# Kernel tuning notes

Hardware: AMD Instinct MI355X
Metric: run time of the kernel (lower is better)

## Reference

```python
import jax, jax.numpy as jnp
import numpy as np

H = 1024      # hidden_size
M = 64        # matrix_dim = int(sqrt(4096))
R = 2         # rank
LS = 2048     # local_size = budget_size // 2


def setup_inputs() -> dict:
    key = jax.random.key(0)
    ks = jax.random.split(key, 12)
    B, S = 4, 2048
    def lin(k, fan_in, fan_out):
        # stored as [in, out] so forward is x @ W
        return jax.random.normal(k, (fan_in, fan_out), dtype=jnp.float32) / np.sqrt(fan_in)
    return {
        "x": jax.random.normal(ks[0], (B, S, H), dtype=jnp.float32),
        "W_decay": lin(ks[1], H, 1),
        "W_key": lin(ks[2], H, R * M),
        "W_value": lin(ks[3], H, R * M),
        "W_ql": lin(ks[4], H, M),
        "W_qr": lin(ks[5], H, M),
        "W_rec_out": lin(ks[6], M, H),
        "W_up": lin(ks[7], H, LS),
        "W_gate": lin(ks[8], H, LS),
        "W_down": lin(ks[9], LS, H),
        "init_state": jnp.zeros((M, M), dtype=jnp.float32),
    }


def reference(x, W_decay, W_key, W_value, W_ql, W_qr, W_rec_out, W_up, W_gate, W_down, init_state):
    B, S, _ = x.shape
    # Precompute all per-token projections (vectorized over batch & seq)
    decay = jax.nn.sigmoid(x @ W_decay)[..., 0]            # [B,S]
    keys = (x @ W_key).reshape(B, S, R, M)                 # [B,S,R,M]
    values = (x @ W_value).reshape(B, S, R, M)             # [B,S,R,M]
    write = jnp.einsum('bsrm,bsrn->bsmn', keys, values) / float(R)  # [B,S,M,M]
    ql = x @ W_ql                                          # [B,S,M]
    qr = x @ W_qr                                          # [B,S,M]

    def step(state, inp):
        d, w, ql_t, qr_t = inp                             # d:[B], w:[B,M,M], ql/qr:[B,M]
        d3 = d[:, None, None]
        state = d3 * state + (1.0 - d3) * w                # decayed matrix-state update
        read = jnp.einsum('bm,bmn->bn', ql_t, state) * qr_t  # [B,M]
        return state, read

    state0 = jnp.broadcast_to(init_state, (B, M, M))
    # scan over time axis (time-major inputs)
    _, reads = jax.lax.scan(
        step, state0,
        (decay.transpose(1, 0), write.transpose(1, 0, 2, 3),
         ql.transpose(1, 0, 2), qr.transpose(1, 0, 2)))
    reads = reads.transpose(1, 0, 2)                       # [B,S,M]

    recurrent = jax.nn.silu(reads) @ W_rec_out             # [B,S,H]
    local = ((x @ W_up) * jax.nn.silu(x @ W_gate)) @ W_down  # SwiGLU branch
    return recurrent + local
```

## Files before the change

kernel.cpp:

```cpp
#include <hip/hip_runtime.h>
#include <hip/hip_bf16.h>

typedef __bf16 bf16x8 __attribute__((ext_vector_type(8)));
typedef float f32x4 __attribute__((ext_vector_type(4)));

#define BS   8192
#define Hd   1024
#define LSd  2048
#define Md   64

static __device__ __forceinline__ float bfu2f(unsigned short u) {
  return __uint_as_float(((unsigned int)u) << 16);
}
static __device__ __forceinline__ __hip_bfloat16 f2bf(float f) { return __float2bfloat16(f); }



__global__ __launch_bounds__(256) void conv_frag_kernel(const float* __restrict__ src,
    __hip_bfloat16* __restrict__ dst) {
  int wid = (blockIdx.x * 256 + threadIdx.x) >> 6;
  int lane = threadIdx.x & 63;
  int t = wid >> 3, ri = wid & 7;
  int mb = t >> 5, kt = t & 31;
  int row = mb * 128 + ri * 16 + (lane & 15);
  int k = kt * 32 + (lane >> 4) * 8;
  const float* s = src + (size_t)row * 1024 + k;
  float4 f0 = *(const float4*)s;
  float4 f1 = *(const float4*)(s + 4);
  union { unsigned short u8[8]; uint4 v; } o;
  o.u8[0] = __bfloat16_as_ushort(f2bf(f0.x)); o.u8[1] = __bfloat16_as_ushort(f2bf(f0.y));
  o.u8[2] = __bfloat16_as_ushort(f2bf(f0.z)); o.u8[3] = __bfloat16_as_ushort(f2bf(f0.w));
  o.u8[4] = __bfloat16_as_ushort(f2bf(f1.x)); o.u8[5] = __bfloat16_as_ushort(f2bf(f1.y));
  o.u8[6] = __bfloat16_as_ushort(f2bf(f1.z)); o.u8[7] = __bfloat16_as_ushort(f2bf(f1.w));
  *(uint4*)(dst + (size_t)wid * 512 + lane * 8) = o.v;
}

__global__ __launch_bounds__(256) void prep_wcat_frag_kernel(const float* __restrict__ Wd,
    const float* __restrict__ Wk, const float* __restrict__ Wv,
    const float* __restrict__ Wql, const float* __restrict__ Wqr,
    __hip_bfloat16* __restrict__ out) {
  int i = blockIdx.x * 256 + threadIdx.x;
  int t = i >> 12, ri = (i >> 9) & 7, l = (i >> 3) & 63, e = i & 7;
  int n = (t >> 5) * 128 + ri * 16 + (l & 15);
  int h = (t & 31) * 32 + (l >> 4) * 8 + e;
  float v = 0.f;
  if (n == 0)        v = Wd[h];
  else if (n < 129)  v = Wk[h * 128 + (n - 1)];
  else if (n < 257)  v = Wv[h * 128 + (n - 129)];
  else if (n < 321)  v = Wql[h * 64 + (n - 257)];
  else if (n < 385)  v = Wqr[h * 64 + (n - 321)];
  out[i] = f2bf(v);
}

__global__ __launch_bounds__(256) void transpose_all_kernel(
    const float* __restrict__ Wup, const float* __restrict__ Wgate,
    const float* __restrict__ Wdown, const float* __restrict__ Wrec,
    __hip_bfloat16* __restrict__ Wug_f, __hip_bfloat16* __restrict__ Wdn_f,
    __hip_bfloat16* __restrict__ Wrc_f) {
  __shared__ float tile[32][129];
  int b = blockIdx.x;
  const float* src; __hip_bfloat16* dst; int Ktot, Nsrc, n_off, kt, nb;
  if (b < 512)        { src = Wup;   dst = Wug_f; Ktot = 1024; Nsrc = 2048; n_off = 0;    int r = b;        kt = r & 31; nb = r >> 5; }
  else if (b < 1024)  { src = Wgate; dst = Wug_f; Ktot = 1024; Nsrc = 2048; n_off = 2048; int r = b - 512;  kt = r & 31; nb = r >> 5; }
  else if (b < 1536)  { src = Wdown; dst = Wdn_f; Ktot = 2048; Nsrc = 1024; n_off = 0;    int r = b - 1024; kt = r & 63; nb = r >> 6; }
  else                { src = Wrec;  dst = Wrc_f; Ktot = 64;   Nsrc = 1024; n_off = 0;    int r = b - 1536; kt = r & 1;  nb = r >> 1; }
  int k0 = kt * 32, n0 = nb * 128;
  int tid = threadIdx.x;
  int kr = tid >> 3, nc = (tid & 7) * 16;
  const float* s = src + (size_t)(k0 + kr) * Nsrc + n0 + nc;
  #pragma unroll
  for (int u = 0; u < 16; u += 4) {
    float4 f = *(const float4*)(s + u);
    tile[kr][nc + u + 0] = f.x; tile[kr][nc + u + 1] = f.y;
    tile[kr][nc + u + 2] = f.z; tile[kr][nc + u + 3] = f.w;
  }
  __syncthreads();
  int wave = tid >> 6, lane = tid & 63;
  int tIdx = ((n0 + n_off) >> 7) * (Ktot >> 5) + kt;
  __hip_bfloat16* d = dst + ((size_t)tIdx << 12);
  #pragma unroll
  for (int it = 0; it < 2; ++it) {
    int ri = wave * 2 + it;
    int nl = ri * 16 + (lane & 15), kq = (lane >> 4) * 8;
    union { unsigned short u8[8]; uint4 v; } o;
    #pragma unroll
    for (int e = 0; e < 8; ++e)
      o.u8[e] = __bfloat16_as_ushort(f2bf(tile[kq + e][nl]));
    *(uint4*)(d + ri * 512 + lane * 8) = o.v;
  }
}


static __device__ __forceinline__ void stage_async_frag(const __hip_bfloat16* __restrict__ tile_src,
    __hip_bfloat16* __restrict__ dst, int wave, int lane) {
  #pragma unroll
  for (int it = 0; it < 2; ++it) {
    int ri = wave * 2 + it;
    __builtin_amdgcn_global_load_lds(
        (const __attribute__((address_space(1))) void*)(tile_src + ri * 512 + lane * 8),
        (__attribute__((address_space(3))) void*)(dst + ri * 512),
        16, 0, 0);
  }
}

static __device__ __forceinline__ void mfma_single(const __hip_bfloat16* sA, const __hip_bfloat16* sB,
    int wm16, int wn16, int lane, f32x4 acc[4][4]) {
  bf16x8 af[4], bg[4];
  #pragma unroll
  for (int i = 0; i < 4; ++i) af[i] = *(const bf16x8*)(sA + (wm16 + i) * 512 + lane * 8);
  #pragma unroll
  for (int j = 0; j < 4; ++j) bg[j] = *(const bf16x8*)(sB + (wn16 + j) * 512 + lane * 8);
  #pragma unroll
  for (int i = 0; i < 4; ++i)
    #pragma unroll
    for (int j = 0; j < 4; ++j)
      acc[i][j] = __builtin_amdgcn_mfma_f32_16x16x32_bf16(af[i], bg[j], acc[i][j], 0, 0, 0);
}

static __device__ __forceinline__ void mfma_dual(const __hip_bfloat16* sA,
    const __hip_bfloat16* sBu, const __hip_bfloat16* sBg,
    int wm16, int wn16, int lane, f32x4 accu[4][4], f32x4 accg[4][4]) {
  bf16x8 af[4], bu[4], bg[4];
  #pragma unroll
  for (int i = 0; i < 4; ++i) af[i] = *(const bf16x8*)(sA + (wm16 + i) * 512 + lane * 8);
  #pragma unroll
  for (int j = 0; j < 4; ++j) bu[j] = *(const bf16x8*)(sBu + (wn16 + j) * 512 + lane * 8);
  #pragma unroll
  for (int j = 0; j < 4; ++j) bg[j] = *(const bf16x8*)(sBg + (wn16 + j) * 512 + lane * 8);
  #pragma unroll
  for (int i = 0; i < 4; ++i)
    #pragma unroll
    for (int j = 0; j < 4; ++j) {
      accu[i][j] = __builtin_amdgcn_mfma_f32_16x16x32_bf16(af[i], bu[j], accu[i][j], 0, 0, 0);
      accg[i][j] = __builtin_amdgcn_mfma_f32_16x16x32_bf16(af[i], bg[j], accg[i][j], 0, 0, 0);
    }
}

__global__ __launch_bounds__(256, 2) void gemm_proj_kernel(const __hip_bfloat16* __restrict__ A,
    const __hip_bfloat16* __restrict__ Bt, float* __restrict__ C) {
  __shared__ __align__(16) __hip_bfloat16 sA[8192];
  __shared__ __align__(16) __hip_bfloat16 sB[8192];
  int tid = threadIdx.x, mb = blockIdx.x, nb = blockIdx.y;
  int wave = tid >> 6, lane = tid & 63;
  int wm16 = (wave >> 1) * 4, wn16 = (wave & 1) * 4;
  int fr = lane & 15, q4 = (lane >> 4) * 4;
  f32x4 acc[4][4] = {};
  for (int kt = 0; kt < 32; kt += 2) {
    __syncthreads();
    stage_async_frag(A + ((size_t)(mb * 32 + kt) << 12), sA, wave, lane);
    stage_async_frag(A + ((size_t)(mb * 32 + kt + 1) << 12), sA + 4096, wave, lane);
    stage_async_frag(Bt + ((size_t)(nb * 32 + kt) << 12), sB, wave, lane);
    stage_async_frag(Bt + ((size_t)(nb * 32 + kt + 1) << 12), sB + 4096, wave, lane);
    __syncthreads();
    mfma_single(sA, sB, wm16, wn16, lane, acc);
    mfma_single(sA + 4096, sB + 4096, wm16, wn16, lane, acc);
  }
  #pragma unroll
  for (int i = 0; i < 4; ++i)
    #pragma unroll
    for (int j = 0; j < 4; ++j) {
      int row = mb * 128 + (wm16 + i) * 16 + q4;
      int col = nb * 128 + (wn16 + j) * 16 + fr;
      #pragma unroll
      for (int rg = 0; rg < 4; ++rg)
        C[(size_t)(row + rg) * 512 + col] = acc[i][j][rg];
    }
}

__global__ __launch_bounds__(256, 2) void gemm_upgate_kernel(const __hip_bfloat16* __restrict__ A,
    const __hip_bfloat16* __restrict__ Bt, __hip_bfloat16* __restrict__ hout) {
  __shared__ __align__(16) __hip_bfloat16 sA[8192];
  __shared__ __align__(16) __hip_bfloat16 sBu[8192];
  __shared__ __align__(16) __hip_bfloat16 sBg[8192];
  int tid = threadIdx.x, mb = blockIdx.x, nb = blockIdx.y;
  int wave = tid >> 6, lane = tid & 63;
  int wm16 = (wave >> 1) * 4, wn16 = (wave & 1) * 4;
  int fr = lane & 15, q4 = (lane >> 4) * 4;
  f32x4 accu[4][4] = {}, accg[4][4] = {};
  for (int kt = 0; kt < 32; kt += 2) {
    __syncthreads();
    stage_async_frag(A + ((size_t)(mb * 32 + kt) << 12), sA, wave, lane);
    stage_async_frag(A + ((size_t)(mb * 32 + kt + 1) << 12), sA + 4096, wave, lane);
    stage_async_frag(Bt + ((size_t)(nb * 32 + kt) << 12), sBu, wave, lane);
    stage_async_frag(Bt + ((size_t)(nb * 32 + kt + 1) << 12), sBu + 4096, wave, lane);
    stage_async_frag(Bt + ((size_t)((nb + 16) * 32 + kt) << 12), sBg, wave, lane);
    stage_async_frag(Bt + ((size_t)((nb + 16) * 32 + kt + 1) << 12), sBg + 4096, wave, lane);
    __syncthreads();
    mfma_dual(sA, sBu, sBg, wm16, wn16, lane, accu, accg);
    mfma_dual(sA + 4096, sBu + 4096, sBg + 4096, wm16, wn16, lane, accu, accg);
  }
  #pragma unroll
  for (int i = 0; i < 4; ++i)
    #pragma unroll
    for (int j = 0; j < 4; ++j) {
      int col = nb * 128 + (wn16 + j) * 16 + fr;
      int q = (col >> 3) & 3, e = col & 7;
      size_t base = ((size_t)(mb * 64 + (col >> 5)) << 12) + (wm16 + i) * 512 + q * 128 + e;
      #pragma unroll
      for (int rg = 0; rg < 4; ++rg) {
        float u = accu[i][j][rg], g = accg[i][j][rg];
        float hv = u * g / (1.f + __expf(-g));
        hout[base + (q4 + rg) * 8] = f2bf(hv);
      }
    }
}

__global__ __launch_bounds__(256, 2) void gemm_final_kernel(const __hip_bfloat16* __restrict__ A,
    const __hip_bfloat16* __restrict__ Bt, const __hip_bfloat16* __restrict__ A2,
    const __hip_bfloat16* __restrict__ B2t, float* __restrict__ C) {
  __shared__ __align__(16) __hip_bfloat16 sA[8192];
  __shared__ __align__(16) __hip_bfloat16 sB[8192];
  int tid = threadIdx.x, mb = blockIdx.x, nb = blockIdx.y;
  int wave = tid >> 6, lane = tid & 63;
  int wm16 = (wave >> 1) * 4, wn16 = (wave & 1) * 4;
  int fr = lane & 15, q4 = (lane >> 4) * 4;
  f32x4 acc[4][4] = {};
  for (int kt = 0; kt < 64; kt += 2) {
    __syncthreads();
    stage_async_frag(A + ((size_t)(mb * 64 + kt) << 12), sA, wave, lane);
    stage_async_frag(A + ((size_t)(mb * 64 + kt + 1) << 12), sA + 4096, wave, lane);
    stage_async_frag(Bt + ((size_t)(nb * 64 + kt) << 12), sB, wave, lane);
    stage_async_frag(Bt + ((size_t)(nb * 64 + kt + 1) << 12), sB + 4096, wave, lane);
    __syncthreads();
    mfma_single(sA, sB, wm16, wn16, lane, acc);
    mfma_single(sA + 4096, sB + 4096, wm16, wn16, lane, acc);
  }
  {
    __syncthreads();
    stage_async_frag(A2 + ((size_t)(mb * 2) << 12), sA, wave, lane);
    stage_async_frag(A2 + ((size_t)(mb * 2 + 1) << 12), sA + 4096, wave, lane);
    stage_async_frag(B2t + ((size_t)(nb * 2) << 12), sB, wave, lane);
    stage_async_frag(B2t + ((size_t)(nb * 2 + 1) << 12), sB + 4096, wave, lane);
    __syncthreads();
    mfma_single(sA, sB, wm16, wn16, lane, acc);
    mfma_single(sA + 4096, sB + 4096, wm16, wn16, lane, acc);
  }
  #pragma unroll
  for (int i = 0; i < 4; ++i)
    #pragma unroll
    for (int j = 0; j < 4; ++j) {
      int row = mb * 128 + (wm16 + i) * 16 + q4;
      int col = nb * 128 + (wn16 + j) * 16 + fr;
      #pragma unroll
      for (int rg = 0; rg < 4; ++rg)
        C[(size_t)(row + rg) * Hd + col] = acc[i][j][rg];
    }
}


__global__ __launch_bounds__(256) void scan_chunk_kernel(const float* __restrict__ proj,
    float* __restrict__ Lam, float* __restrict__ udv, float* __restrict__ alpha,
    float* __restrict__ dS) {
  int bc = blockIdx.x, t0 = bc * 64, tid = threadIdx.x;
  __shared__ float d_s[64], ld_s[64], Lam_s[64], u_s[64];
  __shared__ __align__(16) __hip_bfloat16 k_s[128 * 64];
  __shared__ __align__(16) __hip_bfloat16 v_s[128 * 64];
  if (tid < 64) {
    float z = proj[(size_t)(t0 + tid) * 512];
    float dd = 1.f / (1.f + __expf(-z));
    float l = (z >= 0.f) ? -log1pf(__expf(-z)) : (z - log1pf(__expf(z)));
    d_s[tid] = dd; ld_s[tid] = l;
  }
  __syncthreads();
  if (tid == 0) {
    float s = 0.f;
    for (int j = 0; j < 64; ++j) { s += ld_s[j]; Lam_s[j] = s; }
  }
  __syncthreads();
  float Lend = Lam_s[63];
  if (tid < 64) {
    u_s[tid] = (1.f - d_s[tid]) * __expf(Lend - Lam_s[tid]) * 0.5f;
    Lam[t0 + tid] = Lam_s[tid];
    udv[t0 + tid] = (1.f - d_s[tid]) * 0.5f;
  }
  if (tid == 0) alpha[bc] = __expf(Lend);
  __syncthreads();
  for (int i = tid; i < 128 * 64; i += 256) {
    int jr = i >> 6, m = i & 63, j = jr >> 1, r = jr & 1;
    const float* rowp = proj + (size_t)(t0 + j) * 512;
    k_s[i] = f2bf(u_s[j] * rowp[1 + r * 64 + m]);
    v_s[i] = f2bf(rowp[129 + r * 64 + m]);
  }
  __syncthreads();
  int m0 = (tid & 15) * 4, n0 = (tid >> 4) * 4;
  float acc[4][4] = {{0.f}};
  for (int jr = 0; jr < 128; ++jr) {
    ushort4 ku = *(const ushort4*)&k_s[jr * 64 + m0];
    ushort4 vu = *(const ushort4*)&v_s[jr * 64 + n0];
    float k0 = bfu2f(ku.x), k1 = bfu2f(ku.y), k2 = bfu2f(ku.z), k3 = bfu2f(ku.w);
    float v0 = bfu2f(vu.x), v1 = bfu2f(vu.y), v2 = bfu2f(vu.z), v3 = bfu2f(vu.w);
    acc[0][0] += k0 * v0; acc[0][1] += k0 * v1; acc[0][2] += k0 * v2; acc[0][3] += k0 * v3;
    acc[1][0] += k1 * v0; acc[1][1] += k1 * v1; acc[1][2] += k1 * v2; acc[1][3] += k1 * v3;
    acc[2][0] += k2 * v0; acc[2][1] += k2 * v1; acc[2][2] += k2 * v2; acc[2][3] += k2 * v3;
    acc[3][0] += k3 * v0; acc[3][1] += k3 * v1; acc[3][2] += k3 * v2; acc[3][3] += k3 * v3;
  }
  float* outp = dS + (size_t)bc * 4096;
  #pragma unroll
  for (int a = 0; a < 4; ++a)
    #pragma unroll
    for (int b2 = 0; b2 < 4; ++b2)
      outp[(m0 + a) * 64 + (n0 + b2)] = acc[a][b2];
}

__global__ __launch_bounds__(256) void scan_cross_kernel(const float* __restrict__ dS,
    const float* __restrict__ alpha, const float* __restrict__ init_state,
    float* __restrict__ Sin) {
  int idx = blockIdx.x * 256 + threadIdx.x;
  int b = idx >> 12, e = idx & 4095;
  float s = init_state[e];
  for (int c = 0; c < 32; ++c) {
    int bc = b * 32 + c;
    Sin[(size_t)bc * 4096 + e] = s;
    s = alpha[bc] * s + dS[(size_t)bc * 4096 + e];
  }
}

#define QLD 68

__global__ __launch_bounds__(256) void scan_read_kernel(const float* __restrict__ proj,
    const float* __restrict__ Lam, const float* __restrict__ udv,
    const float* __restrict__ Sin, __hip_bfloat16* __restrict__ Rd) {
  int bc = blockIdx.x, t0 = bc * 64, tid = threadIdx.x;
  __shared__ __align__(16) __hip_bfloat16 ql_s[64 * QLD];
  __shared__ __align__(16) __hip_bfloat16 kv_s[128 * 64];
  __shared__ __align__(16) __hip_bfloat16 S_s[64 * 64];
  __shared__ __align__(16) __hip_bfloat16 P_s[128 * 64];
  __shared__ float Lam_s[64], ud_s[64], eL_s[64];
  for (int i = tid; i < 64 * 64; i += 256) {
    int t = i >> 6, m = i & 63;
    ql_s[t * QLD + m] = f2bf(proj[(size_t)(t0 + t) * 512 + 257 + m]);
    S_s[i] = f2bf(Sin[(size_t)bc * 4096 + i]);
  }
  for (int i = tid; i < 128 * 64; i += 256) {
    int jr = i >> 6, m = i & 63, j = jr >> 1, r = jr & 1;
    kv_s[i] = f2bf(proj[(size_t)(t0 + j) * 512 + 1 + r * 64 + m]);
  }
  if (tid < 64) {
    float L = Lam[t0 + tid];
    Lam_s[tid] = L; ud_s[tid] = udv[t0 + tid]; eL_s[tid] = __expf(L);
  }
  __syncthreads();
  int tr = (tid & 15) * 4, n0 = (tid >> 4) * 4;
  float acc[4][4] = {{0.f}};
  for (int mb4 = 0; mb4 < 64; mb4 += 4) {
    float sm[4][4];
    #pragma unroll
    for (int mm = 0; mm < 4; ++mm) {
      ushort4 sv = *(const ushort4*)&S_s[(mb4 + mm) * 64 + n0];
      sm[mm][0] = bfu2f(sv.x); sm[mm][1] = bfu2f(sv.y);
      sm[mm][2] = bfu2f(sv.z); sm[mm][3] = bfu2f(sv.w);
    }
    #pragma unroll
    for (int a = 0; a < 4; ++a) {
      ushort4 qa = *(const ushort4*)&ql_s[(tr + a) * QLD + mb4];
      float q0 = bfu2f(qa.x), q1 = bfu2f(qa.y), q2 = bfu2f(qa.z), q3 = bfu2f(qa.w);
      #pragma unroll
      for (int b2 = 0; b2 < 4; ++b2)
        acc[a][b2] += q0 * sm[0][b2] + q1 * sm[1][b2] + q2 * sm[2][b2] + q3 * sm[3][b2];
    }
  }
  #pragma unroll
  for (int a = 0; a < 4; ++a) {
    float e = eL_s[tr + a];
    #pragma unroll
    for (int b2 = 0; b2 < 4; ++b2) acc[a][b2] *= e;
  }
  {
    int jr = tid >> 1, j = jr >> 1, tb = (tid & 1) * 32;
    float dot[32];
    #pragma unroll
    for (int t2 = 0; t2 < 32; ++t2) dot[t2] = 0.f;
    for (int m = 0; m < 64; m += 4) {
      ushort4 kb = *(const ushort4*)&kv_s[jr * 64 + m];
      float k0 = bfu2f(kb.x), k1 = bfu2f(kb.y), k2 = bfu2f(kb.z), k3 = bfu2f(kb.w);
      #pragma unroll
      for (int t2 = 0; t2 < 32; ++t2) {
        ushort4 qa = *(const ushort4*)&ql_s[(tb + t2) * QLD + m];
        dot[t2] += bfu2f(qa.x) * k0 + bfu2f(qa.y) * k1 + bfu2f(qa.z) * k2 + bfu2f(qa.w) * k3;
      }
    }
    #pragma unroll
    for (int t2 = 0; t2 < 32; ++t2) {
      int t = tb + t2;
      float coef = (j <= t) ? ud_s[j] * __expf(Lam_s[t] - Lam_s[j]) : 0.f;
      P_s[jr * 64 + t] = f2bf(dot[t2] * coef);
    }
  }
  __syncthreads();
  for (int i = tid; i < 128 * 64; i += 256) {
    int jr = i >> 6, m = i & 63, j = jr >> 1, r = jr & 1;
    kv_s[i] = f2bf(proj[(size_t)(t0 + j) * 512 + 129 + r * 64 + m]);
  }
  __syncthreads();
  for (int jr = 0; jr < 128; ++jr) {
    ushort4 pu = *(const ushort4*)&P_s[jr * 64 + tr];
    ushort4 vu = *(const ushort4*)&kv_s[jr * 64 + n0];
    float p0 = bfu2f(pu.x), p1 = bfu2f(pu.y), p2 = bfu2f(pu.z), p3 = bfu2f(pu.w);
    float v0 = bfu2f(vu.x), v1 = bfu2f(vu.y), v2 = bfu2f(vu.z), v3 = bfu2f(vu.w);
    acc[0][0] += p0 * v0; acc[0][1] += p0 * v1; acc[0][2] += p0 * v2; acc[0][3] += p0 * v3;
    acc[1][0] += p1 * v0; acc[1][1] += p1 * v1; acc[1][2] += p1 * v2; acc[1][3] += p1 * v3;
    acc[2][0] += p2 * v0; acc[2][1] += p2 * v1; acc[2][2] += p2 * v2; acc[2][3] += p2 * v3;
    acc[3][0] += p3 * v0; acc[3][1] += p3 * v1; acc[3][2] += p3 * v2; acc[3][3] += p3 * v3;
  }
  #pragma unroll
  for (int a = 0; a < 4; ++a) {
    int row = t0 + tr + a;
    const float* qrp = proj + (size_t)row * 512 + 321;
    int tBase = (row >> 7) * 2, ri = (row >> 4) & 7, rl = row & 15;
    #pragma unroll
    for (int b2 = 0; b2 < 4; ++b2) {
      int n = n0 + b2;
      float rv = acc[a][b2] * qrp[n];
      float sv = rv / (1.f + __expf(-rv));
      size_t idx = ((size_t)(tBase + (n >> 5)) << 12) + ri * 512
                 + (rl + ((n >> 3) & 3) * 16) * 8 + (n & 7);
      Rd[idx] = f2bf(sv);
    }
  }
}


extern "C" void kernel_launch(void* const* d_in, const int* in_sizes, int n_in,
                              void* d_out, int out_size, void* d_ws, size_t ws_size,
                              hipStream_t stream) {
  const float* x      = (const float*)d_in[0];
  const float* W_dec  = (const float*)d_in[1];
  const float* W_key  = (const float*)d_in[2];
  const float* W_val  = (const float*)d_in[3];
  const float* W_ql   = (const float*)d_in[4];
  const float* W_qr   = (const float*)d_in[5];
  const float* W_rec  = (const float*)d_in[6];
  const float* W_up   = (const float*)d_in[7];
  const float* W_gate = (const float*)d_in[8];
  const float* W_down = (const float*)d_in[9];
  const float* init_state = (const float*)d_in[10];
  float* out = (float*)d_out;

  char* w = (char*)d_ws;
  auto take = [&](size_t bytes) { char* p = w; w += (bytes + 255) & ~(size_t)255; return p; };
  __hip_bfloat16* x_fb   = (__hip_bfloat16*)take((size_t)BS * Hd * 2);
  __hip_bfloat16* Wcat_f = (__hip_bfloat16*)take((size_t)512 * Hd * 2);
  __hip_bfloat16* Wug_f  = (__hip_bfloat16*)take((size_t)4096 * Hd * 2);
  __hip_bfloat16* Wdn_f  = (__hip_bfloat16*)take((size_t)Hd * LSd * 2);
  __hip_bfloat16* Wrc_f  = (__hip_bfloat16*)take((size_t)Hd * Md * 2);
  float* proj  = (float*)take((size_t)BS * 512 * 4);
  float* Lam   = (float*)take((size_t)BS * 4);
  float* udv   = (float*)take((size_t)BS * 4);
  float* alpha = (float*)take((size_t)128 * 4);
  float* dS    = (float*)take((size_t)128 * 4096 * 4);
  float* Sin   = (float*)take((size_t)128 * 4096 * 4);
  __hip_bfloat16* Rd   = (__hip_bfloat16*)take((size_t)BS * Md * 2);
  __hip_bfloat16* hbuf = (__hip_bfloat16*)take((size_t)BS * LSd * 2);

  conv_frag_kernel<<<4096, 256, 0, stream>>>(x, x_fb);
  prep_wcat_frag_kernel<<<2048, 256, 0, stream>>>(W_dec, W_key, W_val, W_ql, W_qr, Wcat_f);
  transpose_all_kernel<<<1552, 256, 0, stream>>>(W_up, W_gate, W_down, W_rec,
                                                 Wug_f, Wdn_f, Wrc_f);

  gemm_proj_kernel<<<dim3(64, 4), 256, 0, stream>>>(x_fb, Wcat_f, proj);

  scan_chunk_kernel<<<128, 256, 0, stream>>>(proj, Lam, udv, alpha, dS);
  scan_cross_kernel<<<64, 256, 0, stream>>>(dS, alpha, init_state, Sin);
  scan_read_kernel<<<128, 256, 0, stream>>>(proj, Lam, udv, Sin, Rd);

  gemm_upgate_kernel<<<dim3(64, 16), 256, 0, stream>>>(x_fb, Wug_f, hbuf);
  gemm_final_kernel<<<dim3(64, 8), 256, 0, stream>>>(hbuf, Wdn_f, Rd, Wrc_f, out);
}
```

Measured before the change: 301.7 us.

## Merge prep kernels, fold cross-chunk state scan into read kernel, shuffle prefix sum

Merges the three weight and input conversion kernels into one launch of 7696 blocks that branches on block index. Removes the separate cross-chunk scan kernel and its Sin buffer: each read block now rebuilds its own starting state by replaying all earlier chunks' decay and dS contributions in registers. The serial single-thread prefix sum over log-decay becomes a wave shuffle scan. This saves two launches and a global round trip, at the cost of redundant cross-chunk work that grows with the chunk index, so later blocks do more work than earlier ones.

```diff
diff --git a/kernel.cpp b/kernel.cpp
--- a/kernel.cpp
+++ b/kernel.cpp
@@ -16,77 +16,76 @@
 
 
 
-__global__ __launch_bounds__(256) void conv_frag_kernel(const float* __restrict__ src,
-    __hip_bfloat16* __restrict__ dst) {
-  int wid = (blockIdx.x * 256 + threadIdx.x) >> 6;
-  int lane = threadIdx.x & 63;
-  int t = wid >> 3, ri = wid & 7;
-  int mb = t >> 5, kt = t & 31;
-  int row = mb * 128 + ri * 16 + (lane & 15);
-  int k = kt * 32 + (lane >> 4) * 8;
-  const float* s = src + (size_t)row * 1024 + k;
-  float4 f0 = *(const float4*)s;
-  float4 f1 = *(const float4*)(s + 4);
-  union { unsigned short u8[8]; uint4 v; } o;
-  o.u8[0] = __bfloat16_as_ushort(f2bf(f0.x)); o.u8[1] = __bfloat16_as_ushort(f2bf(f0.y));
-  o.u8[2] = __bfloat16_as_ushort(f2bf(f0.z)); o.u8[3] = __bfloat16_as_ushort(f2bf(f0.w));
-  o.u8[4] = __bfloat16_as_ushort(f2bf(f1.x)); o.u8[5] = __bfloat16_as_ushort(f2bf(f1.y));
-  o.u8[6] = __bfloat16_as_ushort(f2bf(f1.z)); o.u8[7] = __bfloat16_as_ushort(f2bf(f1.w));
-  *(uint4*)(dst + (size_t)wid * 512 + lane * 8) = o.v;
-}
-
-__global__ __launch_bounds__(256) void prep_wcat_frag_kernel(const float* __restrict__ Wd,
-    const float* __restrict__ Wk, const float* __restrict__ Wv,
-    const float* __restrict__ Wql, const float* __restrict__ Wqr,
-    __hip_bfloat16* __restrict__ out) {
-  int i = blockIdx.x * 256 + threadIdx.x;
-  int t = i >> 12, ri = (i >> 9) & 7, l = (i >> 3) & 63, e = i & 7;
-  int n = (t >> 5) * 128 + ri * 16 + (l & 15);
-  int h = (t & 31) * 32 + (l >> 4) * 8 + e;
-  float v = 0.f;
-  if (n == 0)        v = Wd[h];
-  else if (n < 129)  v = Wk[h * 128 + (n - 1)];
-  else if (n < 257)  v = Wv[h * 128 + (n - 129)];
-  else if (n < 321)  v = Wql[h * 64 + (n - 257)];
-  else if (n < 385)  v = Wqr[h * 64 + (n - 321)];
-  out[i] = f2bf(v);
-}
-
-__global__ __launch_bounds__(256) void transpose_all_kernel(
+__global__ __launch_bounds__(256) void prep_all_kernel(
+    const float* __restrict__ x,
+    const float* __restrict__ Wd, const float* __restrict__ Wk,
+    const float* __restrict__ Wv, const float* __restrict__ Wql,
+    const float* __restrict__ Wqr,
     const float* __restrict__ Wup, const float* __restrict__ Wgate,
     const float* __restrict__ Wdown, const float* __restrict__ Wrec,
+    __hip_bfloat16* __restrict__ x_fb, __hip_bfloat16* __restrict__ Wcat_f,
     __hip_bfloat16* __restrict__ Wug_f, __hip_bfloat16* __restrict__ Wdn_f,
     __hip_bfloat16* __restrict__ Wrc_f) {
   __shared__ float tile[32][129];
-  int b = blockIdx.x;
-  const float* src; __hip_bfloat16* dst; int Ktot, Nsrc, n_off, kt, nb;
-  if (b < 512)        { src = Wup;   dst = Wug_f; Ktot = 1024; Nsrc = 2048; n_off = 0;    int r = b;        kt = r & 31; nb = r >> 5; }
-  else if (b < 1024)  { src = Wgate; dst = Wug_f; Ktot = 1024; Nsrc = 2048; n_off = 2048; int r = b - 512;  kt = r & 31; nb = r >> 5; }
-  else if (b < 1536)  { src = Wdown; dst = Wdn_f; Ktot = 2048; Nsrc = 1024; n_off = 0;    int r = b - 1024; kt = r & 63; nb = r >> 6; }
-  else                { src = Wrec;  dst = Wrc_f; Ktot = 64;   Nsrc = 1024; n_off = 0;    int r = b - 1536; kt = r & 1;  nb = r >> 1; }
-  int k0 = kt * 32, n0 = nb * 128;
-  int tid = threadIdx.x;
-  int kr = tid >> 3, nc = (tid & 7) * 16;
-  const float* s = src + (size_t)(k0 + kr) * Nsrc + n0 + nc;
-  #pragma unroll
-  for (int u = 0; u < 16; u += 4) {
-    float4 f = *(const float4*)(s + u);
-    tile[kr][nc + u + 0] = f.x; tile[kr][nc + u + 1] = f.y;
-    tile[kr][nc + u + 2] = f.z; tile[kr][nc + u + 3] = f.w;
-  }
-  __syncthreads();
-  int wave = tid >> 6, lane = tid & 63;
-  int tIdx = ((n0 + n_off) >> 7) * (Ktot >> 5) + kt;
-  __hip_bfloat16* d = dst + ((size_t)tIdx << 12);
-  #pragma unroll
-  for (int it = 0; it < 2; ++it) {
-    int ri = wave * 2 + it;
-    int nl = ri * 16 + (lane & 15), kq = (lane >> 4) * 8;
+  int b = blockIdx.x, tid = threadIdx.x;
+  if (b < 4096) {
+    int wid = (b * 256 + tid) >> 6;
+    int lane = tid & 63;
+    int t = wid >> 3, ri = wid & 7;
+    int mb = t >> 5, kt = t & 31;
+    int row = mb * 128 + ri * 16 + (lane & 15);
+    int k = kt * 32 + (lane >> 4) * 8;
+    const float* s = x + (size_t)row * 1024 + k;
+    float4 f0 = *(const float4*)s;
+    float4 f1 = *(const float4*)(s + 4);
     union { unsigned short u8[8]; uint4 v; } o;
-    #pragma unroll
-    for (int e = 0; e < 8; ++e)
-      o.u8[e] = __bfloat16_as_ushort(f2bf(tile[kq + e][nl]));
-    *(uint4*)(d + ri * 512 + lane * 8) = o.v;
+    o.u8[0] = __bfloat16_as_ushort(f2bf(f0.x)); o.u8[1] = __bfloat16_as_ushort(f2bf(f0.y));
+    o.u8[2] = __bfloat16_as_ushort(f2bf(f0.z)); o.u8[3] = __bfloat16_as_ushort(f2bf(f0.w));
+    o.u8[4] = __bfloat16_as_ushort(f2bf(f1.x)); o.u8[5] = __bfloat16_as_ushort(f2bf(f1.y));
+    o.u8[6] = __bfloat16_as_ushort(f2bf(f1.z)); o.u8[7] = __bfloat16_as_ushort(f2bf(f1.w));
+    *(uint4*)(x_fb + (size_t)wid * 512 + lane * 8) = o.v;
+  } else if (b < 6144) {
+    int i = (b - 4096) * 256 + tid;
+    int t = i >> 12, ri = (i >> 9) & 7, l = (i >> 3) & 63, e = i & 7;
+    int n = (t >> 5) * 128 + ri * 16 + (l & 15);
+    int h = (t & 31) * 32 + (l >> 4) * 8 + e;
+    float v = 0.f;
+    if (n == 0)        v = Wd[h];
+    else if (n < 129)  v = Wk[h * 128 + (n - 1)];
+    else if (n < 257)  v = Wv[h * 128 + (n - 129)];
+    else if (n < 321)  v = Wql[h * 64 + (n - 257)];
+    else if (n < 385)  v = Wqr[h * 64 + (n - 321)];
+    Wcat_f[i] = f2bf(v);
+  } else {
+    int bb = b - 6144;
+    const float* src; __hip_bfloat16* dst; int Ktot, Nsrc, n_off, kt, nb;
+    if (bb < 512)        { src = Wup;   dst = Wug_f; Ktot = 1024; Nsrc = 2048; n_off = 0;    int r = bb;        kt = r & 31; nb = r >> 5; }
+    else if (bb < 1024)  { src = Wgate; dst = Wug_f; Ktot = 1024; Nsrc = 2048; n_off = 2048; int r = bb - 512;  kt = r & 31; nb = r >> 5; }
+    else if (bb < 1536)  { src = Wdown; dst = Wdn_f; Ktot = 2048; Nsrc = 1024; n_off = 0;    int r = bb - 1024; kt = r & 63; nb = r >> 6; }
+    else                 { src = Wrec;  dst = Wrc_f; Ktot = 64;   Nsrc = 1024; n_off = 0;    int r = bb - 1536; kt = r & 1;  nb = r >> 1; }
+    int k0 = kt * 32, n0 = nb * 128;
+    int kr = tid >> 3, nc = (tid & 7) * 16;
+    const float* s = src + (size_t)(k0 + kr) * Nsrc + n0 + nc;
+    #pragma unroll
+    for (int u = 0; u < 16; u += 4) {
+      float4 f = *(const float4*)(s + u);
+      tile[kr][nc + u + 0] = f.x; tile[kr][nc + u + 1] = f.y;
+      tile[kr][nc + u + 2] = f.z; tile[kr][nc + u + 3] = f.w;
+    }
+    __syncthreads();
+    int wave = tid >> 6, lane = tid & 63;
+    int tIdx = ((n0 + n_off) >> 7) * (Ktot >> 5) + kt;
+    __hip_bfloat16* d = dst + ((size_t)tIdx << 12);
+    #pragma unroll
+    for (int it = 0; it < 2; ++it) {
+      int ri = wave * 2 + it;
+      int nl = ri * 16 + (lane & 15), kq = (lane >> 4) * 8;
+      union { unsigned short u8[8]; uint4 v; } o;
+      #pragma unroll
+      for (int e = 0; e < 8; ++e)
+        o.u8[e] = __bfloat16_as_ushort(f2bf(tile[kq + e][nl]));
+      *(uint4*)(d + ri * 512 + lane * 8) = o.v;
+    }
   }
 }
 
@@ -252,28 +251,28 @@
     float* __restrict__ Lam, float* __restrict__ udv, float* __restrict__ alpha,
     float* __restrict__ dS) {
   int bc = blockIdx.x, t0 = bc * 64, tid = threadIdx.x;
-  __shared__ float d_s[64], ld_s[64], Lam_s[64], u_s[64];
+  __shared__ float Lam_s[64], u_s[64];
   __shared__ __align__(16) __hip_bfloat16 k_s[128 * 64];
   __shared__ __align__(16) __hip_bfloat16 v_s[128 * 64];
+  float dd = 0.f, v = 0.f;
   if (tid < 64) {
     float z = proj[(size_t)(t0 + tid) * 512];
-    float dd = 1.f / (1.f + __expf(-z));
+    dd = 1.f / (1.f + __expf(-z));
     float l = (z >= 0.f) ? -log1pf(__expf(-z)) : (z - log1pf(__expf(z)));
-    d_s[tid] = dd; ld_s[tid] = l;
-  }
-  __syncthreads();
-  if (tid == 0) {
-    float s = 0.f;
-    for (int j = 0; j < 64; ++j) { s += ld_s[j]; Lam_s[j] = s; }
+    v = l;
+    #pragma unroll
+    for (int off = 1; off < 64; off <<= 1) {
+      float o = __shfl_up(v, off, 64);
+      if (tid >= off) v += o;
+    }
+    Lam_s[tid] = v;
+    Lam[t0 + tid] = v;
+    udv[t0 + tid] = (1.f - dd) * 0.5f;
+    if (tid == 63) alpha[bc] = __expf(v);
   }
   __syncthreads();
   float Lend = Lam_s[63];
-  if (tid < 64) {
-    u_s[tid] = (1.f - d_s[tid]) * __expf(Lend - Lam_s[tid]) * 0.5f;
-    Lam[t0 + tid] = Lam_s[tid];
-    udv[t0 + tid] = (1.f - d_s[tid]) * 0.5f;
-  }
-  if (tid == 0) alpha[bc] = __expf(Lend);
+  if (tid < 64) u_s[tid] = (1.f - dd) * __expf(Lend - v) * 0.5f;
   __syncthreads();
   for (int i = tid; i < 128 * 64; i += 256) {
     int jr = i >> 6, m = i & 63, j = jr >> 1, r = jr & 1;
@@ -302,34 +301,35 @@
       outp[(m0 + a) * 64 + (n0 + b2)] = acc[a][b2];
 }
 
-__global__ __launch_bounds__(256) void scan_cross_kernel(const float* __restrict__ dS,
-    const float* __restrict__ alpha, const float* __restrict__ init_state,
-    float* __restrict__ Sin) {
-  int idx = blockIdx.x * 256 + threadIdx.x;
-  int b = idx >> 12, e = idx & 4095;
-  float s = init_state[e];
-  for (int c = 0; c < 32; ++c) {
-    int bc = b * 32 + c;
-    Sin[(size_t)bc * 4096 + e] = s;
-    s = alpha[bc] * s + dS[(size_t)bc * 4096 + e];
-  }
-}
-
 #define QLD 68
 
 __global__ __launch_bounds__(256) void scan_read_kernel(const float* __restrict__ proj,
     const float* __restrict__ Lam, const float* __restrict__ udv,
-    const float* __restrict__ Sin, __hip_bfloat16* __restrict__ Rd) {
+    const float* __restrict__ dS, const float* __restrict__ alpha,
+    const float* __restrict__ init_state, __hip_bfloat16* __restrict__ Rd) {
   int bc = blockIdx.x, t0 = bc * 64, tid = threadIdx.x;
   __shared__ __align__(16) __hip_bfloat16 ql_s[64 * QLD];
   __shared__ __align__(16) __hip_bfloat16 kv_s[128 * 64];
   __shared__ __align__(16) __hip_bfloat16 S_s[64 * 64];
   __shared__ __align__(16) __hip_bfloat16 P_s[128 * 64];
   __shared__ float Lam_s[64], ud_s[64], eL_s[64];
+  {
+    int b = bc >> 5, c = bc & 31;
+    float sreg[16];
+    #pragma unroll
+    for (int k = 0; k < 16; ++k) sreg[k] = init_state[tid + k * 256];
+    for (int cp = 0; cp < c; ++cp) {
+      float a = alpha[b * 32 + cp];
+      const float* dsp = dS + (size_t)(b * 32 + cp) * 4096;
+      #pragma unroll
+      for (int k = 0; k < 16; ++k) sreg[k] = a * sreg[k] + dsp[tid + k * 256];
+    }
+    #pragma unroll
+    for (int k = 0; k < 16; ++k) S_s[tid + k * 256] = f2bf(sreg[k]);
+  }
   for (int i = tid; i < 64 * 64; i += 256) {
     int t = i >> 6, m = i & 63;
     ql_s[t * QLD + m] = f2bf(proj[(size_t)(t0 + t) * 512 + 257 + m]);
-    S_s[i] = f2bf(Sin[(size_t)bc * 4096 + i]);
   }
   for (int i = tid; i < 128 * 64; i += 256) {
     int jr = i >> 6, m = i & 63, j = jr >> 1, r = jr & 1;
@@ -448,20 +448,17 @@
   float* udv   = (float*)take((size_t)BS * 4);
   float* alpha = (float*)take((size_t)128 * 4);
   float* dS    = (float*)take((size_t)128 * 4096 * 4);
-  float* Sin   = (float*)take((size_t)128 * 4096 * 4);
   __hip_bfloat16* Rd   = (__hip_bfloat16*)take((size_t)BS * Md * 2);
   __hip_bfloat16* hbuf = (__hip_bfloat16*)take((size_t)BS * LSd * 2);
 
-  conv_frag_kernel<<<4096, 256, 0, stream>>>(x, x_fb);
-  prep_wcat_frag_kernel<<<2048, 256, 0, stream>>>(W_dec, W_key, W_val, W_ql, W_qr, Wcat_f);
-  transpose_all_kernel<<<1552, 256, 0, stream>>>(W_up, W_gate, W_down, W_rec,
-                                                 Wug_f, Wdn_f, Wrc_f);
+  prep_all_kernel<<<7696, 256, 0, stream>>>(x, W_dec, W_key, W_val, W_ql, W_qr,
+                                            W_up, W_gate, W_down, W_rec,
+                                            x_fb, Wcat_f, Wug_f, Wdn_f, Wrc_f);
 
   gemm_proj_kernel<<<dim3(64, 4), 256, 0, stream>>>(x_fb, Wcat_f, proj);
 
   scan_chunk_kernel<<<128, 256, 0, stream>>>(proj, Lam, udv, alpha, dS);
-  scan_cross_kernel<<<64, 256, 0, stream>>>(dS, alpha, init_state, Sin);
-  scan_read_kernel<<<128, 256, 0, stream>>>(proj, Lam, udv, Sin, Rd);
+  scan_read_kernel<<<128, 256, 0, stream>>>(proj, Lam, udv, dS, alpha, init_state, Rd);
 
   gemm_upgate_kernel<<<dim3(64, 16), 256, 0, stream>>>(x_fb, Wug_f, hbuf);
   gemm_final_kernel<<<dim3(64, 8), 256, 0, stream>>>(hbuf, Wdn_f, Rd, Wrc_f, out);
```

Result: faster. 295.2 us (-2.1%).
